# Kernel optimization log

Measured on AMD Instinct MI355X. Metric: run time of the kernel, lower is better.

Reference implementation:

```python
import jax, jax.numpy as jnp
import numpy as np

DEPTH = 3
N = 32768          # total nodes
G = 256            # num graphs
P = N // G         # nodes per graph (last node is the virtual node)
E = 524288         # edges
IN, H, H2 = 8, 64, 128


def _lin(key, out_d, in_d):
    w = jax.random.normal(key, (out_d, in_d), dtype=jnp.float32) * (1.0 / np.sqrt(in_d))
    b = jnp.zeros((out_d,), dtype=jnp.float32)
    return w, b


def setup_inputs() -> dict:
    key = jax.random.key(0)
    ks = jax.random.split(key, 10)
    x = jax.random.normal(ks[0], (N, IN), dtype=jnp.float32)
    edge_index = jax.random.randint(ks[1], (2, E), 0, N, dtype=jnp.int32).astype(jnp.int64)
    batch = (jnp.arange(N, dtype=jnp.int64) // P)
    W1, b1 = _lin(ks[2], H, IN)
    W2, b2 = _lin(ks[3], H, H)
    W3, b3 = _lin(ks[4], H, H)
    W4, b4 = _lin(ks[5], H, 2 * H)
    W5, b5 = _lin(ks[6], H, H * H)
    Wd1, bd1 = _lin(ks[7], H2, H)
    Wd2, bd2 = _lin(ks[8], 1, H2)
    return {"x": x, "edge_index": edge_index, "batch": batch, "num_graphs": G,
            "W1": W1, "b1": b1, "W2": W2, "b2": b2, "W3": W3, "b3": b3,
            "W4": W4, "b4": b4, "W5": W5, "b5": b5,
            "Wd1": Wd1, "bd1": bd1, "Wd2": Wd2, "bd2": bd2}


def reference(x, edge_index, batch, num_graphs,
              W1, b1, W2, b2, W3, b3, W4, b4, W5, b5, Wd1, bd1, Wd2, bd2):
    # initial embed: linear -> relu -> L2 normalize
    h = jax.nn.relu(x @ W1.T + b1)
    h = h / jnp.linalg.norm(h, axis=-1, keepdims=True)
    src, dst = edge_index[0], edge_index[1]
    for _ in range(DEPTH):
        # sum-aggregate neighbor messages (PyG add aggregation: gather src, scatter-add to dst)
        m = jax.ops.segment_sum(h[src], dst, num_segments=N)
        cat = jnp.concatenate([m @ W3.T + b3, h @ W2.T + b2], axis=-1)  # [N, 2H]
        h = jax.nn.relu(cat @ W4.T + b4)
        h = h / jnp.linalg.norm(h, axis=-1, keepdims=True)
    # per-graph: outer product of each non-virtual node embedding with the
    # last (virtual) node embedding. Graphs are equal-sized -> vectorize by reshape.
    hg = h.reshape(num_graphs, P, H)
    others = hg[:, :-1, :]          # [G, P-1, H]
    last = hg[:, -1, :]             # [G, H]
    outer = jnp.einsum('gpi,gj->gpij', others, last)        # [G, P-1, H, H]
    outer = outer.reshape(num_graphs * (P - 1), H * H)       # flatten(start_dim=1), row-major i*H+j
    y = outer @ W5.T + b5
    y = jax.nn.relu(y @ Wd1.T + bd1)
    y = y @ Wd2.T + bd2              # [G*(P-1), 1] Q-values
    return y
```

## Files before the change

kernel.cpp:

```cpp
#include <hip/hip_runtime.h>
#include <hip/hip_bf16.h>

#define NN 32768
#define EE 524288
#define GG 256
#define PP 128

__global__ void k_init(const float* __restrict__ x, const float* __restrict__ W1,
                       const float* __restrict__ b1,
                       const float* __restrict__ W2, const float* __restrict__ b2,
                       const float* __restrict__ W3, const float* __restrict__ b3,
                       const float* __restrict__ W4, const float* __restrict__ b4,
                       const float* __restrict__ Wd1,
                       float* __restrict__ h0, float* __restrict__ h1,
                       float* __restrict__ Wc, float* __restrict__ Wd1t,
                       int* __restrict__ deg, int* __restrict__ csr) {
    __shared__ float tile[128 * 65];
    int b = blockIdx.x, t = threadIdx.x;
    if (b >= 8192) {
        if (b == 8224) {
            for (int idx = t; idx < 8192; idx += 256) {
                int q = idx >> 6, o = idx & 63;
                tile[q*65 + o] = Wd1[idx];
            }
            __syncthreads();
            for (int idx = t; idx < 8192; idx += 256) {
                int o = idx >> 7, q = idx & 127;
                Wd1t[idx] = tile[q*65 + o];
            }
        } else if (b == 8225) {
            if (t < 64)       h0[(long)NN*64 + t] = 0.f;
            else if (t < 128) h1[(long)NN*64 + (t-64)] = 0.f;
        } else {
            int idx = (b - 8192) * 256 + t;
            int kk = idx >> 6, o = idx & 63;
            float a = 0.f;
            if (kk < 64) {
                for (int j = 0; j < 64; ++j) a += W4[o*128 + j] * W3[j*64 + kk];
            } else {
                int k2 = kk - 64;
                for (int j = 0; j < 64; ++j) a += W4[o*128 + 64 + j] * W2[j*64 + k2];
            }
            Wc[kk*64 + o] = a;
            if (idx < 64) {
                float c = b4[idx];
                for (int j = 0; j < 64; ++j)
                    c += W4[idx*128 + j]*b3[j] + W4[idx*128 + 64 + j]*b2[j];
                Wc[8192 + idx] = c;
            }
        }
        return;
    }
    if (b < 128) deg[b * 256 + t] = 0;
    if (t < 64)
        ((int4*)csr)[b*64 + t] = make_int4(NN, NN, NN, NN);
    int node = (b * 256 + t) >> 6;
    int lane = t & 63;
    float acc = b1[lane];
    #pragma unroll
    for (int j = 0; j < 8; ++j)
        acc += x[node*8 + j] * W1[lane*8 + j];
    acc = fmaxf(acc, 0.f);
    float ss = acc * acc;
    #pragma unroll
    for (int m = 1; m < 64; m <<= 1) ss += __shfl_xor(ss, m, 64);
    h0[node*64 + lane] = acc / sqrtf(ss);
}

__global__ void k_fill(const int* __restrict__ src, const int* __restrict__ dst,
                       int* __restrict__ deg, int* __restrict__ csr) {
    int i = blockIdx.x * blockDim.x + threadIdx.x;
    int4 s4 = ((const int4*)src)[i];
    int4 d4 = ((const int4*)dst)[i];
    csr[(d4.x << 6) + atomicAdd(&deg[d4.x], 1)] = s4.x;
    csr[(d4.y << 6) + atomicAdd(&deg[d4.y], 1)] = s4.y;
    csr[(d4.z << 6) + atomicAdd(&deg[d4.z], 1)] = s4.z;
    csr[(d4.w << 6) + atomicAdd(&deg[d4.w], 1)] = s4.w;
}

__global__ void __launch_bounds__(256) k_gather(
        const float* __restrict__ h, const int* __restrict__ deg,
        const int* __restrict__ csr, float* __restrict__ m) {
    int node = (blockIdx.x * blockDim.x + threadIdx.x) >> 6;
    int lane = threadIdx.x & 63;
    int fg4 = (lane & 15) * 4, es = lane >> 4;
    int dg = __builtin_amdgcn_readfirstlane(deg[node]);
    int de4 = (dg + 3) >> 2;
    const int4* csr4 = (const int4*)csr + node * 16;
    float4 acc = make_float4(0.f, 0.f, 0.f, 0.f);
    for (int q = es; q < de4; q += 4) {
        int4 idx = csr4[q];
        float4 v0 = *(const float4*)&h[(long)idx.x*64 + fg4];
        float4 v1 = *(const float4*)&h[(long)idx.y*64 + fg4];
        float4 v2 = *(const float4*)&h[(long)idx.z*64 + fg4];
        float4 v3 = *(const float4*)&h[(long)idx.w*64 + fg4];
        acc.x += (v0.x + v1.x) + (v2.x + v3.x);
        acc.y += (v0.y + v1.y) + (v2.y + v3.y);
        acc.z += (v0.z + v1.z) + (v2.z + v3.z);
        acc.w += (v0.w + v1.w) + (v2.w + v3.w);
    }
    acc.x += __shfl_xor(acc.x, 16, 64); acc.y += __shfl_xor(acc.y, 16, 64);
    acc.z += __shfl_xor(acc.z, 16, 64); acc.w += __shfl_xor(acc.w, 16, 64);
    acc.x += __shfl_xor(acc.x, 32, 64); acc.y += __shfl_xor(acc.y, 32, 64);
    acc.z += __shfl_xor(acc.z, 32, 64); acc.w += __shfl_xor(acc.w, 32, 64);
    if (es == 0) *(float4*)&m[(long)node*64 + fg4] = acc;
}

__global__ void __launch_bounds__(256) k_gemm(
        const float* __restrict__ Wc, float* mio,
        const float* __restrict__ hcur) {
    __shared__ float Wl[8192];
    __shared__ float Xl[64 * 132];
    int t = threadIdx.x;
    int nbase = blockIdx.x * 64;

    for (int i = t * 4; i < 8192; i += 1024)
        *(float4*)&Wl[i] = *(const float4*)&Wc[i];
    for (int idx = t; idx < 1024; idx += 256) {
        int n = idx >> 4, c = (idx & 15) * 4;
        *(float4*)&Xl[n*132 + c]      = *(const float4*)&mio[(long)(nbase+n)*64 + c];
        *(float4*)&Xl[n*132 + 64 + c] = *(const float4*)&hcur[(long)(nbase+n)*64 + c];
    }
    __syncthreads();

    int tc = t & 15, tr = t >> 4;
    int o0 = tc * 4, n0 = tr * 4;
    float4 c4 = *(const float4*)&Wc[8192 + o0];
    float acc[4][4] = {};
    #pragma unroll 2
    for (int kk = 0; kk < 128; kk += 4) {
        float4 w0 = *(float4*)&Wl[(kk+0)*64 + o0];
        float4 w1 = *(float4*)&Wl[(kk+1)*64 + o0];
        float4 w2 = *(float4*)&Wl[(kk+2)*64 + o0];
        float4 w3 = *(float4*)&Wl[(kk+3)*64 + o0];
        #pragma unroll
        for (int jn = 0; jn < 4; ++jn) {
            float4 xv = *(float4*)&Xl[(n0+jn)*132 + kk];
            acc[jn][0] += xv.x*w0.x + xv.y*w1.x + xv.z*w2.x + xv.w*w3.x;
            acc[jn][1] += xv.x*w0.y + xv.y*w1.y + xv.z*w2.y + xv.w*w3.y;
            acc[jn][2] += xv.x*w0.z + xv.y*w1.z + xv.z*w2.z + xv.w*w3.z;
            acc[jn][3] += xv.x*w0.w + xv.y*w1.w + xv.z*w2.w + xv.w*w3.w;
        }
    }

    #pragma unroll
    for (int jn = 0; jn < 4; ++jn) {
        float v0 = fmaxf(acc[jn][0] + c4.x, 0.f);
        float v1 = fmaxf(acc[jn][1] + c4.y, 0.f);
        float v2 = fmaxf(acc[jn][2] + c4.z, 0.f);
        float v3 = fmaxf(acc[jn][3] + c4.w, 0.f);
        float ss = v0*v0 + v1*v1 + v2*v2 + v3*v3;
        ss += __shfl_xor(ss, 1, 64);
        ss += __shfl_xor(ss, 2, 64);
        ss += __shfl_xor(ss, 4, 64);
        ss += __shfl_xor(ss, 8, 64);
        float r = 1.0f / sqrtf(ss);
        float4 outv = make_float4(v0*r, v1*r, v2*r, v3*r);
        *(float4*)&mio[(long)(nbase + n0 + jn)*64 + o0] = outv;
    }
}

__global__ void __launch_bounds__(256) k_tmat(
        const float* __restrict__ h, const float* __restrict__ W5,
        float* __restrict__ Tt) {
    __shared__ float lastL[256 * 65];
    __shared__ float wL[64 * 16];
    __shared__ float tr[16 * 257];
    int t = threadIdx.x;
    int rb = blockIdx.x * 16;
    int i = rb >> 6, obase = rb & 63;

    for (int idx4 = t; idx4 < 4096; idx4 += 256) {
        int g = idx4 >> 4, c = (idx4 & 15) * 4;
        *(float4*)&lastL[g*65 + c] =
            *(const float4*)&h[((long)g*128 + 127)*64 + c];
    }
    {
        int rr = t & 15, j0 = (t >> 4) * 4;
        float4 w = *(const float4*)&W5[(long)(obase + rr)*4096 + i*64 + j0];
        wL[(j0+0)*16 + rr] = w.x;
        wL[(j0+1)*16 + rr] = w.y;
        wL[(j0+2)*16 + rr] = w.z;
        wL[(j0+3)*16 + rr] = w.w;
    }
    __syncthreads();

    int g = t;
    float acc[16] = {};
    for (int j = 0; j < 64; ++j) {
        float lv = lastL[g*65 + j];
        #pragma unroll
        for (int r4 = 0; r4 < 4; ++r4) {
            float4 wv = *(float4*)&wL[j*16 + r4*4];
            acc[r4*4+0] += wv.x * lv;
            acc[r4*4+1] += wv.y * lv;
            acc[r4*4+2] += wv.z * lv;
            acc[r4*4+3] += wv.w * lv;
        }
    }
    #pragma unroll
    for (int rr = 0; rr < 16; ++rr) tr[rr*257 + g] = acc[rr];
    __syncthreads();
    for (int it = 0; it < 4; ++it) {
        int idx = t + it*256;
        int g2 = idx >> 2, c4 = idx & 3;
        float4 v = make_float4(tr[(c4*4+0)*257 + g2], tr[(c4*4+1)*257 + g2],
                               tr[(c4*4+2)*257 + g2], tr[(c4*4+3)*257 + g2]);
        *(float4*)&Tt[(long)g2*4096 + rb + c4*4] = v;
    }
}

__global__ void __launch_bounds__(256) k_readout(
        const float* __restrict__ h, const float* __restrict__ Tt,
        const float* __restrict__ b5, const float* __restrict__ Wd1t,
        const float* __restrict__ bd1, const float* __restrict__ Wd2,
        const float* __restrict__ bd2, float* __restrict__ out) {
    __shared__ float Tl[4096];
    __shared__ float W1t[8192];
    __shared__ float OY[32 * 68];
    int t = threadIdx.x;
    int g = blockIdx.x;

    for (int i = t * 4; i < 4096; i += 1024)
        *(float4*)&Tl[i] = *(const float4*)&Tt[(long)g*4096 + i];
    for (int i = t * 4; i < 8192; i += 1024)
        *(float4*)&W1t[i] = *(const float4*)&Wd1t[i];

    int tc = t & 15, tr = t >> 4;
    int o0 = tc * 4, p0 = tr * 2;
    int tc2 = t & 31, tr2 = t >> 5;
    int q0 = tc2 * 4, pp0 = tr2 * 4;
    float4 b5_4  = *(const float4*)&b5[o0];
    float4 bd1_4 = *(const float4*)&bd1[q0];
    float4 wd2_4 = *(const float4*)&Wd2[q0];
    float bd2v = bd2[0];

    for (int pt = 0; pt < 4; ++pt) {
        int pbase = pt * 32;
        __syncthreads();
        for (int idx = t; idx < 512; idx += 256) {
            int p = idx >> 4, c = (idx & 15) * 4;
            *(float4*)&OY[p*68 + c] =
                *(const float4*)&h[((long)g*128 + pbase + p)*64 + c];
        }
        __syncthreads();

        float a10[4] = {0.f,0.f,0.f,0.f};
        float a11[4] = {0.f,0.f,0.f,0.f};
        #pragma unroll 4
        for (int i = 0; i < 64; i += 4) {
            float4 w0 = *(float4*)&Tl[(i+0)*64 + o0];
            float4 w1 = *(float4*)&Tl[(i+1)*64 + o0];
            float4 w2 = *(float4*)&Tl[(i+2)*64 + o0];
            float4 w3 = *(float4*)&Tl[(i+3)*64 + o0];
            float4 x0 = *(float4*)&OY[(p0+0)*68 + i];
            float4 x1 = *(float4*)&OY[(p0+1)*68 + i];
            a10[0] += x0.x*w0.x + x0.y*w1.x + x0.z*w2.x + x0.w*w3.x;
            a10[1] += x0.x*w0.y + x0.y*w1.y + x0.z*w2.y + x0.w*w3.y;
            a10[2] += x0.x*w0.z + x0.y*w1.z + x0.z*w2.z + x0.w*w3.z;
            a10[3] += x0.x*w0.w + x0.y*w1.w + x0.z*w2.w + x0.w*w3.w;
            a11[0] += x1.x*w0.x + x1.y*w1.x + x1.z*w2.x + x1.w*w3.x;
            a11[1] += x1.x*w0.y + x1.y*w1.y + x1.z*w2.y + x1.w*w3.y;
            a11[2] += x1.x*w0.z + x1.y*w1.z + x1.z*w2.z + x1.w*w3.z;
            a11[3] += x1.x*w0.w + x1.y*w1.w + x1.z*w2.w + x1.w*w3.w;
        }
        __syncthreads();

        float4 y0 = make_float4(a10[0]+b5_4.x, a10[1]+b5_4.y, a10[2]+b5_4.z, a10[3]+b5_4.w);
        float4 y1 = make_float4(a11[0]+b5_4.x, a11[1]+b5_4.y, a11[2]+b5_4.z, a11[3]+b5_4.w);
        *(float4*)&OY[(p0+0)*68 + o0] = y0;
        *(float4*)&OY[(p0+1)*68 + o0] = y1;
        __syncthreads();

        float a2[4][4] = {};
        #pragma unroll 4
        for (int o = 0; o < 64; o += 4) {
            float4 w0 = *(float4*)&W1t[(o+0)*128 + q0];
            float4 w1 = *(float4*)&W1t[(o+1)*128 + q0];
            float4 w2 = *(float4*)&W1t[(o+2)*128 + q0];
            float4 w3 = *(float4*)&W1t[(o+3)*128 + q0];
            #pragma unroll
            for (int jp = 0; jp < 4; ++jp) {
                float4 yv = *(float4*)&OY[(pp0+jp)*68 + o];
                a2[jp][0] += yv.x*w0.x + yv.y*w1.x + yv.z*w2.x + yv.w*w3.x;
                a2[jp][1] += yv.x*w0.y + yv.y*w1.y + yv.z*w2.y + yv.w*w3.y;
                a2[jp][2] += yv.x*w0.z + yv.y*w1.z + yv.z*w2.z + yv.w*w3.z;
                a2[jp][3] += yv.x*w0.w + yv.y*w1.w + yv.z*w2.w + yv.w*w3.w;
            }
        }

        #pragma unroll
        for (int jp = 0; jp < 4; ++jp) {
            float s = wd2_4.x * fmaxf(a2[jp][0] + bd1_4.x, 0.f)
                    + wd2_4.y * fmaxf(a2[jp][1] + bd1_4.y, 0.f)
                    + wd2_4.z * fmaxf(a2[jp][2] + bd1_4.z, 0.f)
                    + wd2_4.w * fmaxf(a2[jp][3] + bd1_4.w, 0.f);
            s += __shfl_xor(s, 1, 64);
            s += __shfl_xor(s, 2, 64);
            s += __shfl_xor(s, 4, 64);
            s += __shfl_xor(s, 8, 64);
            s += __shfl_xor(s, 16, 64);
            if (tc2 == 0) {
                int p = pbase + pp0 + jp;
                if (p < 127) out[g*127 + p] = s + bd2v;
            }
        }
    }
}

extern "C" void kernel_launch(void* const* d_in, const int* in_sizes, int n_in,
                              void* d_out, int out_size, void* d_ws, size_t ws_size,
                              hipStream_t stream) {
    const float* x   = (const float*)d_in[0];
    const int*   ei  = (const int*)d_in[1];
    const float* W1  = (const float*)d_in[4];
    const float* b1  = (const float*)d_in[5];
    const float* W2  = (const float*)d_in[6];
    const float* b2  = (const float*)d_in[7];
    const float* W3  = (const float*)d_in[8];
    const float* b3  = (const float*)d_in[9];
    const float* W4  = (const float*)d_in[10];
    const float* b4  = (const float*)d_in[11];
    const float* W5  = (const float*)d_in[12];
    const float* b5  = (const float*)d_in[13];
    const float* Wd1 = (const float*)d_in[14];
    const float* bd1 = (const float*)d_in[15];
    const float* Wd2 = (const float*)d_in[16];
    const float* bd2 = (const float*)d_in[17];
    float* out = (float*)d_out;

    float* ws  = (float*)d_ws;
    float* h0   = ws;
    float* h1   = ws + 2129984;
    float* Tt   = ws + 4259968;
    float* Wc   = ws + 5308416;
    float* Wd1t = ws + 5316864;
    int*   deg  = (int*)(ws + 5325056);
    int*   csr  = deg + NN;

    const int* src = ei;
    const int* dst = ei + EE;

    k_init<<<8226, 256, 0, stream>>>(x, W1, b1, W2, b2, W3, b3, W4, b4,
                                     Wd1, h0, h1, Wc, Wd1t, deg, csr);
    k_fill<<<512, 256, 0, stream>>>(src, dst, deg, csr);

    float* hc = h0; float* hn = h1;
    for (int l = 0; l < 3; ++l) {
        k_gather<<<NN/4, 256, 0, stream>>>(hc, deg, csr, hn);
        k_gemm<<<NN/64, 256, 0, stream>>>(Wc, hn, hc);
        float* tmp = hc; hc = hn; hn = tmp;
    }

    k_tmat<<<256, 256, 0, stream>>>(hc, W5, Tt);
    k_readout<<<256, 256, 0, stream>>>(hc, Tt, b5, Wd1t, bd1, Wd2, bd2, out);
}
```

Baseline: 273.1 us.

## Fuse neighbor gather into per-layer GEMM kernel, staging aggregates in shared memory

Merges the separate gather and GEMM kernels into one per-layer kernel. Each wave aggregates neighbor features for 16 nodes straight into the shared-memory input tile, so the intermediate message buffer no longer makes a global write and read, and one launch per layer goes away. The gather always loads the first 32 padded CSR slots and prefetches the next node's indices, with an extra loop only for high-degree nodes. This relies on padded CSR entries pointing at a zero row. It also drops gather parallelism from 8192 blocks to 512, which may expose memory latency.

```diff
diff --git a/kernel.cpp b/kernel.cpp
--- a/kernel.cpp
+++ b/kernel.cpp
@@ -78,37 +78,10 @@
     csr[(d4.w << 6) + atomicAdd(&deg[d4.w], 1)] = s4.w;
 }
 
-__global__ void __launch_bounds__(256) k_gather(
-        const float* __restrict__ h, const int* __restrict__ deg,
-        const int* __restrict__ csr, float* __restrict__ m) {
-    int node = (blockIdx.x * blockDim.x + threadIdx.x) >> 6;
-    int lane = threadIdx.x & 63;
-    int fg4 = (lane & 15) * 4, es = lane >> 4;
-    int dg = __builtin_amdgcn_readfirstlane(deg[node]);
-    int de4 = (dg + 3) >> 2;
-    const int4* csr4 = (const int4*)csr + node * 16;
-    float4 acc = make_float4(0.f, 0.f, 0.f, 0.f);
-    for (int q = es; q < de4; q += 4) {
-        int4 idx = csr4[q];
-        float4 v0 = *(const float4*)&h[(long)idx.x*64 + fg4];
-        float4 v1 = *(const float4*)&h[(long)idx.y*64 + fg4];
-        float4 v2 = *(const float4*)&h[(long)idx.z*64 + fg4];
-        float4 v3 = *(const float4*)&h[(long)idx.w*64 + fg4];
-        acc.x += (v0.x + v1.x) + (v2.x + v3.x);
-        acc.y += (v0.y + v1.y) + (v2.y + v3.y);
-        acc.z += (v0.z + v1.z) + (v2.z + v3.z);
-        acc.w += (v0.w + v1.w) + (v2.w + v3.w);
-    }
-    acc.x += __shfl_xor(acc.x, 16, 64); acc.y += __shfl_xor(acc.y, 16, 64);
-    acc.z += __shfl_xor(acc.z, 16, 64); acc.w += __shfl_xor(acc.w, 16, 64);
-    acc.x += __shfl_xor(acc.x, 32, 64); acc.y += __shfl_xor(acc.y, 32, 64);
-    acc.z += __shfl_xor(acc.z, 32, 64); acc.w += __shfl_xor(acc.w, 32, 64);
-    if (es == 0) *(float4*)&m[(long)node*64 + fg4] = acc;
-}
-
-__global__ void __launch_bounds__(256) k_gemm(
-        const float* __restrict__ Wc, float* mio,
-        const float* __restrict__ hcur) {
+__global__ void __launch_bounds__(256) k_layer(
+        const float* __restrict__ Wc, const float* __restrict__ hcur,
+        const int* __restrict__ deg, const int* __restrict__ csr,
+        float* __restrict__ hnext) {
     __shared__ float Wl[8192];
     __shared__ float Xl[64 * 132];
     int t = threadIdx.x;
@@ -118,8 +91,55 @@
         *(float4*)&Wl[i] = *(const float4*)&Wc[i];
     for (int idx = t; idx < 1024; idx += 256) {
         int n = idx >> 4, c = (idx & 15) * 4;
-        *(float4*)&Xl[n*132 + c]      = *(const float4*)&mio[(long)(nbase+n)*64 + c];
         *(float4*)&Xl[n*132 + 64 + c] = *(const float4*)&hcur[(long)(nbase+n)*64 + c];
+    }
+
+    int w = t >> 6, lane = t & 63;
+    int fg4 = (lane & 15) * 4, es = lane >> 4;
+    int nb = nbase + w * 16;
+    int dv = deg[nb + (lane & 15)];
+    const int4* base4 = (const int4*)csr + (long)nb * 16;
+    int4 iA = base4[es];
+    int4 iB = base4[4 + es];
+    for (int ni = 0; ni < 16; ++ni) {
+        int4 cA = iA, cB = iB;
+        if (ni < 15) {
+            iA = base4[(ni+1)*16 + es];
+            iB = base4[(ni+1)*16 + 4 + es];
+        }
+        float4 a0 = *(const float4*)&hcur[(long)cA.x*64 + fg4];
+        float4 a1 = *(const float4*)&hcur[(long)cA.y*64 + fg4];
+        float4 a2 = *(const float4*)&hcur[(long)cA.z*64 + fg4];
+        float4 a3 = *(const float4*)&hcur[(long)cA.w*64 + fg4];
+        float4 b0 = *(const float4*)&hcur[(long)cB.x*64 + fg4];
+        float4 b1 = *(const float4*)&hcur[(long)cB.y*64 + fg4];
+        float4 b2 = *(const float4*)&hcur[(long)cB.z*64 + fg4];
+        float4 b3 = *(const float4*)&hcur[(long)cB.w*64 + fg4];
+        float4 acc;
+        acc.x = ((a0.x + a1.x) + (a2.x + a3.x)) + ((b0.x + b1.x) + (b2.x + b3.x));
+        acc.y = ((a0.y + a1.y) + (a2.y + a3.y)) + ((b0.y + b1.y) + (b2.y + b3.y));
+        acc.z = ((a0.z + a1.z) + (a2.z + a3.z)) + ((b0.z + b1.z) + (b2.z + b3.z));
+        acc.w = ((a0.w + a1.w) + (a2.w + a3.w)) + ((b0.w + b1.w) + (b2.w + b3.w));
+        int dg = __shfl(dv, ni, 64);
+        if (dg > 32) {
+            int de4 = (dg + 3) >> 2;
+            for (int q = es + 8; q < de4; q += 4) {
+                int4 cx = base4[ni*16 + q];
+                float4 v0 = *(const float4*)&hcur[(long)cx.x*64 + fg4];
+                float4 v1 = *(const float4*)&hcur[(long)cx.y*64 + fg4];
+                float4 v2 = *(const float4*)&hcur[(long)cx.z*64 + fg4];
+                float4 v3 = *(const float4*)&hcur[(long)cx.w*64 + fg4];
+                acc.x += (v0.x + v1.x) + (v2.x + v3.x);
+                acc.y += (v0.y + v1.y) + (v2.y + v3.y);
+                acc.z += (v0.z + v1.z) + (v2.z + v3.z);
+                acc.w += (v0.w + v1.w) + (v2.w + v3.w);
+            }
+        }
+        acc.x += __shfl_xor(acc.x, 16, 64); acc.y += __shfl_xor(acc.y, 16, 64);
+        acc.z += __shfl_xor(acc.z, 16, 64); acc.w += __shfl_xor(acc.w, 16, 64);
+        acc.x += __shfl_xor(acc.x, 32, 64); acc.y += __shfl_xor(acc.y, 32, 64);
+        acc.z += __shfl_xor(acc.z, 32, 64); acc.w += __shfl_xor(acc.w, 32, 64);
+        if (es == 0) *(float4*)&Xl[(w*16 + ni)*132 + fg4] = acc;
     }
     __syncthreads();
 
@@ -156,7 +176,7 @@
         ss += __shfl_xor(ss, 8, 64);
         float r = 1.0f / sqrtf(ss);
         float4 outv = make_float4(v0*r, v1*r, v2*r, v3*r);
-        *(float4*)&mio[(long)(nbase + n0 + jn)*64 + o0] = outv;
+        *(float4*)&hnext[(long)(nbase + n0 + jn)*64 + o0] = outv;
     }
 }
 
@@ -347,8 +367,7 @@
 
     float* hc = h0; float* hn = h1;
     for (int l = 0; l < 3; ++l) {
-        k_gather<<<NN/4, 256, 0, stream>>>(hc, deg, csr, hn);
-        k_gemm<<<NN/64, 256, 0, stream>>>(Wc, hn, hc);
+        k_layer<<<NN/64, 256, 0, stream>>>(Wc, hc, deg, csr, hn);
         float* tmp = hc; hc = hn; hn = tmp;
     }
 
```

Measured after the change: 256.8 us. 1.06x faster.
